# Performance work log

Hardware: AMD Instinct MI355X
Metric: run time of the kernel (lower is better)

The kernel has to match this reference:

```python
import jax, jax.numpy as jnp
import numpy as np

G = 7          # grid size
OBJ_P = 0.3    # fraction of cells containing an object


def _to_xyxy(x, y, w, h, m, n):
    # x pairs with grid index m (dim 2), y with n (dim 3), per the original loop
    cx = (x + m) / G
    cy = (y + n) / G
    return cx - w / 2, cy - h / 2, cx + w / 2, cy + h / 2


def _iou(b1, b2):
    x1a, y1a, x2a, y2a = b1
    x1b, y1b, x2b, y2b = b2
    iw = jnp.maximum(jnp.minimum(x2a, x2b) - jnp.maximum(x1a, x1b), 0.0)
    ih = jnp.maximum(jnp.minimum(y2a, y2b) - jnp.maximum(y1a, y1b), 0.0)
    inter = iw * ih
    a1 = (x2a - x1a) * (y2a - y1a)
    a2 = (x2b - x1b) * (y2b - y1b)
    union = a1 + a2 - inter
    return jnp.where(inter > 0, inter / union, 0.0)


def setup_inputs() -> dict:
    key = jax.random.key(0)
    k1, k2, k3 = jax.random.split(key, 3)
    B = 32768
    pred = jax.random.uniform(k1, (B, 30, G, G), dtype=jnp.float32)
    labels = jax.random.uniform(k2, (B, 30, G, G), dtype=jnp.float32)
    obj_mask = jax.random.bernoulli(k3, OBJ_P, (B, G, G)).astype(jnp.float32)
    labels = labels.at[:, 4].set(obj_mask)
    return {"pred": pred, "labels": labels}


def reference(pred, labels):
    B = pred.shape[0]
    m = jnp.arange(G, dtype=pred.dtype)[:, None]   # dim 2
    n = jnp.arange(G, dtype=pred.dtype)[None, :]   # dim 3

    obj = labels[:, 4] == 1.0                       # (B,G,G)

    box1 = _to_xyxy(pred[:, 0], pred[:, 1], pred[:, 2], pred[:, 3], m, n)
    box2 = _to_xyxy(pred[:, 5], pred[:, 6], pred[:, 7], pred[:, 8], m, n)
    boxg = _to_xyxy(labels[:, 0], labels[:, 1], labels[:, 2], labels[:, 3], m, n)

    iou1 = _iou(box1, boxg)
    iou2 = _iou(box2, boxg)
    resp1 = iou1 >= iou2

    coor1 = 5.0 * (jnp.sum((pred[:, 0:2] - labels[:, 0:2]) ** 2, axis=1)
                   + jnp.sum((jnp.sqrt(pred[:, 2:4]) - jnp.sqrt(labels[:, 2:4])) ** 2, axis=1))
    coor2 = 5.0 * (jnp.sum((pred[:, 5:7] - labels[:, 5:7]) ** 2, axis=1)
                   + jnp.sum((jnp.sqrt(pred[:, 7:9]) - jnp.sqrt(labels[:, 7:9])) ** 2, axis=1))

    loss_b1 = coor1 + (pred[:, 4] - iou1) ** 2 + 0.5 * (pred[:, 9] - iou2) ** 2
    loss_b2 = coor2 + (pred[:, 9] - iou2) ** 2 + 0.5 * (pred[:, 4] - iou1) ** 2

    cls = jnp.sum((pred[:, 10:] - labels[:, 10:]) ** 2, axis=1)

    obj_loss = jnp.where(resp1, loss_b1, loss_b2) + cls
    noobj_loss = 0.5 * (pred[:, 4] ** 2 + pred[:, 9] ** 2)

    total = jnp.sum(jnp.where(obj, obj_loss, noobj_loss))
    return total / B
```

## Files before the change

kernel.cpp:

```cpp
#include <hip/hip_runtime.h>


#define GRID 7
#define NCH 30
#define CPI (GRID * GRID)
#define FPI (NCH * CPI)
#define NBLK 2048

__device__ __forceinline__ float iou_xyxy(float x1a, float y1a, float x2a, float y2a,
                                          float x1b, float y1b, float x2b, float y2b) {
    float iw = fmaxf(fminf(x2a, x2b) - fmaxf(x1a, x1b), 0.0f);
    float ih = fmaxf(fminf(y2a, y2b) - fmaxf(y1a, y1b), 0.0f);
    float inter = iw * ih;
    float a1 = (x2a - x1a) * (y2a - y1a);
    float a2 = (x2b - x1b) * (y2b - y1b);
    float uni = a1 + a2 - inter;
    return inter > 0.0f ? inter / uni : 0.0f;
}

__global__ void __launch_bounds__(256) yolo_partial_kernel(
        const float* __restrict__ pred,
        const float* __restrict__ labels,
        float* __restrict__ partials,
        int ncells, float invB) {
    float acc = 0.0f;
    int stride = gridDim.x * blockDim.x;
    for (int idx = blockIdx.x * blockDim.x + threadIdx.x; idx < ncells; idx += stride) {
        int b = idx / CPI;
        int cell = idx - b * CPI;
        int m = cell / GRID;
        int n = cell - m * GRID;

        const float* pb = pred   + (size_t)b * FPI + cell;
        const float* lb = labels + (size_t)b * FPI + cell;

        float p0 = pb[0 * CPI], p1 = pb[1 * CPI], p2 = pb[2 * CPI], p3 = pb[3 * CPI];
        float p4 = pb[4 * CPI], p5 = pb[5 * CPI], p6 = pb[6 * CPI], p7 = pb[7 * CPI];
        float p8 = pb[8 * CPI], p9 = pb[9 * CPI];
        float l0 = lb[0 * CPI], l1 = lb[1 * CPI], l2 = lb[2 * CPI], l3 = lb[3 * CPI];
        float lobj = lb[4 * CPI];
        float l5 = lb[5 * CPI], l6 = lb[6 * CPI], l7 = lb[7 * CPI], l8 = lb[8 * CPI];

        float cls = 0.0f;
        #pragma unroll
        for (int c = 10; c < NCH; ++c) {
            float d = pb[c * CPI] - lb[c * CPI];
            cls += d * d;
        }

        const float inv_g = 1.0f / (float)GRID;
        float fm = (float)m, fn = (float)n;

        float cx = (p0 + fm) * inv_g, cy = (p1 + fn) * inv_g;
        float b1x1 = cx - p2 * 0.5f, b1y1 = cy - p3 * 0.5f;
        float b1x2 = cx + p2 * 0.5f, b1y2 = cy + p3 * 0.5f;
        cx = (p5 + fm) * inv_g; cy = (p6 + fn) * inv_g;
        float b2x1 = cx - p7 * 0.5f, b2y1 = cy - p8 * 0.5f;
        float b2x2 = cx + p7 * 0.5f, b2y2 = cy + p8 * 0.5f;
        cx = (l0 + fm) * inv_g; cy = (l1 + fn) * inv_g;
        float gx1 = cx - l2 * 0.5f, gy1 = cy - l3 * 0.5f;
        float gx2 = cx + l2 * 0.5f, gy2 = cy + l3 * 0.5f;

        float iou1 = iou_xyxy(b1x1, b1y1, b1x2, b1y2, gx1, gy1, gx2, gy2);
        float iou2 = iou_xyxy(b2x1, b2y1, b2x2, b2y2, gx1, gy1, gx2, gy2);
        bool resp1 = iou1 >= iou2;

        float dx = p0 - l0, dy = p1 - l1;
        float dw = sqrtf(p2) - sqrtf(l2), dh = sqrtf(p3) - sqrtf(l3);
        float coor1 = 5.0f * (dx * dx + dy * dy + dw * dw + dh * dh);
        dx = p5 - l5; dy = p6 - l6;
        dw = sqrtf(p7) - sqrtf(l7); dh = sqrtf(p8) - sqrtf(l8);
        float coor2 = 5.0f * (dx * dx + dy * dy + dw * dw + dh * dh);

        float e1 = p4 - iou1, e2 = p9 - iou2;
        float loss_b1 = coor1 + e1 * e1 + 0.5f * e2 * e2;
        float loss_b2 = coor2 + e2 * e2 + 0.5f * e1 * e1;

        float obj_loss = (resp1 ? loss_b1 : loss_b2) + cls;
        float noobj_loss = 0.5f * (p4 * p4 + p9 * p9);

        acc += ((lobj == 1.0f) ? obj_loss : noobj_loss) * invB;
    }

    #pragma unroll
    for (int off = 32; off > 0; off >>= 1)
        acc += __shfl_down(acc, off, 64);

    __shared__ float rsm[4];
    int lane = threadIdx.x & 63;
    int wid = threadIdx.x >> 6;
    if (lane == 0) rsm[wid] = acc;
    __syncthreads();
    if (threadIdx.x == 0)
        partials[blockIdx.x] = rsm[0] + rsm[1] + rsm[2] + rsm[3];
}

__global__ void __launch_bounds__(256) yolo_final_kernel(
        const float* __restrict__ partials, float* __restrict__ out, int n) {
    float acc = 0.0f;
    for (int i = threadIdx.x; i < n; i += 256)
        acc += partials[i];
    #pragma unroll
    for (int off = 32; off > 0; off >>= 1)
        acc += __shfl_down(acc, off, 64);
    __shared__ float rsm[4];
    int lane = threadIdx.x & 63;
    int wid = threadIdx.x >> 6;
    if (lane == 0) rsm[wid] = acc;
    __syncthreads();
    if (threadIdx.x == 0)
        out[0] = rsm[0] + rsm[1] + rsm[2] + rsm[3];
}

extern "C" void kernel_launch(void* const* d_in, const int* in_sizes, int n_in,
                              void* d_out, int out_size, void* d_ws, size_t ws_size,
                              hipStream_t stream) {
    const float* pred = (const float*)d_in[0];
    const float* labels = (const float*)d_in[1];
    float* out = (float*)d_out;
    float* partials = (float*)d_ws;

    int total = in_sizes[0];
    int B = total / FPI;
    int ncells = B * CPI;

    yolo_partial_kernel<<<NBLK, 256, 0, stream>>>(pred, labels, partials,
                                                  ncells, 1.0f / (float)B);
    yolo_final_kernel<<<1, 256, 0, stream>>>(partials, out, NBLK);
}
```

Baseline: 386.4 us.

## Stage per-image tiles into LDS with direct global-to-LDS vector loads

Each block now handles groups of 4 images. It first copies the contiguous pred and label slabs into shared memory with 16-byte global_load_lds transfers. The per-cell loss is then computed from LDS, replacing the 39 strided scalar global loads each thread issued before. Leftover images that do not fill a group are handled in the final reduction kernel, which now sums one partial per group. The cost is about 47KB of LDS per block, which limits occupancy, and roughly a quarter of each block's threads sit idle during compute with no overlap between loading and computing.

```diff
diff --git a/kernel.cpp b/kernel.cpp
--- a/kernel.cpp
+++ b/kernel.cpp
@@ -5,7 +5,15 @@
 #define NCH 30
 #define CPI (GRID * GRID)
 #define FPI (NCH * CPI)
-#define NBLK 2048
+#define IPB 4
+#define BLK 256
+#define CELLS_PB (IPB * CPI)
+#define F_PB (IPB * FPI)
+#define F4_PB (F_PB / 4)
+#define FALLBACK_NBLK 2048
+
+typedef const __attribute__((address_space(1))) void gvoid_t;
+typedef __attribute__((address_space(3))) void lvoid_t;
 
 __device__ __forceinline__ float iou_xyxy(float x1a, float y1a, float x2a, float y2a,
                                           float x1b, float y1b, float x2b, float y2b) {
@@ -18,68 +26,90 @@
     return inter > 0.0f ? inter / uni : 0.0f;
 }
 
-__global__ void __launch_bounds__(256) yolo_partial_kernel(
+__device__ __forceinline__ float cell_loss(const float* __restrict__ pb,
+                                           const float* __restrict__ lb,
+                                           float fm, float fn) {
+    float p0 = pb[0 * CPI], p1 = pb[1 * CPI], p2 = pb[2 * CPI], p3 = pb[3 * CPI];
+    float p4 = pb[4 * CPI], p5 = pb[5 * CPI], p6 = pb[6 * CPI], p7 = pb[7 * CPI];
+    float p8 = pb[8 * CPI], p9 = pb[9 * CPI];
+    float l0 = lb[0 * CPI], l1 = lb[1 * CPI], l2 = lb[2 * CPI], l3 = lb[3 * CPI];
+    float lobj = lb[4 * CPI];
+    float l5 = lb[5 * CPI], l6 = lb[6 * CPI], l7 = lb[7 * CPI], l8 = lb[8 * CPI];
+
+    float cls = 0.0f;
+    #pragma unroll
+    for (int c = 10; c < NCH; ++c) {
+        float d = pb[c * CPI] - lb[c * CPI];
+        cls += d * d;
+    }
+
+    const float inv_g = 1.0f / (float)GRID;
+
+    float cx = (p0 + fm) * inv_g, cy = (p1 + fn) * inv_g;
+    float b1x1 = cx - p2 * 0.5f, b1y1 = cy - p3 * 0.5f;
+    float b1x2 = cx + p2 * 0.5f, b1y2 = cy + p3 * 0.5f;
+    cx = (p5 + fm) * inv_g; cy = (p6 + fn) * inv_g;
+    float b2x1 = cx - p7 * 0.5f, b2y1 = cy - p8 * 0.5f;
+    float b2x2 = cx + p7 * 0.5f, b2y2 = cy + p8 * 0.5f;
+    cx = (l0 + fm) * inv_g; cy = (l1 + fn) * inv_g;
+    float gx1 = cx - l2 * 0.5f, gy1 = cy - l3 * 0.5f;
+    float gx2 = cx + l2 * 0.5f, gy2 = cy + l3 * 0.5f;
+
+    float iou1 = iou_xyxy(b1x1, b1y1, b1x2, b1y2, gx1, gy1, gx2, gy2);
+    float iou2 = iou_xyxy(b2x1, b2y1, b2x2, b2y2, gx1, gy1, gx2, gy2);
+    bool resp1 = iou1 >= iou2;
+
+    float dx = p0 - l0, dy = p1 - l1;
+    float dw = sqrtf(p2) - sqrtf(l2), dh = sqrtf(p3) - sqrtf(l3);
+    float coor1 = 5.0f * (dx * dx + dy * dy + dw * dw + dh * dh);
+    dx = p5 - l5; dy = p6 - l6;
+    dw = sqrtf(p7) - sqrtf(l7); dh = sqrtf(p8) - sqrtf(l8);
+    float coor2 = 5.0f * (dx * dx + dy * dy + dw * dw + dh * dh);
+
+    float e1 = p4 - iou1, e2 = p9 - iou2;
+    float loss_b1 = coor1 + e1 * e1 + 0.5f * e2 * e2;
+    float loss_b2 = coor2 + e2 * e2 + 0.5f * e1 * e1;
+
+    float obj_loss = (resp1 ? loss_b1 : loss_b2) + cls;
+    float noobj_loss = 0.5f * (p4 * p4 + p9 * p9);
+
+    return (lobj == 1.0f) ? obj_loss : noobj_loss;
+}
+
+__global__ void __launch_bounds__(BLK) yolo_partial_kernel(
         const float* __restrict__ pred,
         const float* __restrict__ labels,
         float* __restrict__ partials,
-        int ncells, float invB) {
+        int ngroups, float invB) {
+    __shared__ __align__(16) float sp[F_PB];
+    __shared__ __align__(16) float sl[F_PB];
+
     float acc = 0.0f;
-    int stride = gridDim.x * blockDim.x;
-    for (int idx = blockIdx.x * blockDim.x + threadIdx.x; idx < ncells; idx += stride) {
-        int b = idx / CPI;
-        int cell = idx - b * CPI;
-        int m = cell / GRID;
-        int n = cell - m * GRID;
 
-        const float* pb = pred   + (size_t)b * FPI + cell;
-        const float* lb = labels + (size_t)b * FPI + cell;
+    for (int g = blockIdx.x; g < ngroups; g += gridDim.x) {
+        const float* gp = pred   + (size_t)g * F_PB;
+        const float* gl = labels + (size_t)g * F_PB;
 
-        float p0 = pb[0 * CPI], p1 = pb[1 * CPI], p2 = pb[2 * CPI], p3 = pb[3 * CPI];
-        float p4 = pb[4 * CPI], p5 = pb[5 * CPI], p6 = pb[6 * CPI], p7 = pb[7 * CPI];
-        float p8 = pb[8 * CPI], p9 = pb[9 * CPI];
-        float l0 = lb[0 * CPI], l1 = lb[1 * CPI], l2 = lb[2 * CPI], l3 = lb[3 * CPI];
-        float lobj = lb[4 * CPI];
-        float l5 = lb[5 * CPI], l6 = lb[6 * CPI], l7 = lb[7 * CPI], l8 = lb[8 * CPI];
+        for (int j = threadIdx.x; j < F4_PB; j += BLK)
+            __builtin_amdgcn_global_load_lds((gvoid_t*)(gp + 4 * j),
+                                             (lvoid_t*)(sp + 4 * j), 16, 0, 0);
+        for (int j = threadIdx.x; j < F4_PB; j += BLK)
+            __builtin_amdgcn_global_load_lds((gvoid_t*)(gl + 4 * j),
+                                             (lvoid_t*)(sl + 4 * j), 16, 0, 0);
 
-        float cls = 0.0f;
-        #pragma unroll
-        for (int c = 10; c < NCH; ++c) {
-            float d = pb[c * CPI] - lb[c * CPI];
-            cls += d * d;
+        asm volatile("s_waitcnt vmcnt(0)" ::: "memory");
+        __syncthreads();
+
+        int t = threadIdx.x;
+        if (t < CELLS_PB) {
+            int i = t / CPI;
+            int cell = t - i * CPI;
+            int m = cell / GRID;
+            int n = cell - m * GRID;
+            acc += cell_loss(&sp[i * FPI + cell], &sl[i * FPI + cell],
+                             (float)m, (float)n) * invB;
         }
-
-        const float inv_g = 1.0f / (float)GRID;
-        float fm = (float)m, fn = (float)n;
-
-        float cx = (p0 + fm) * inv_g, cy = (p1 + fn) * inv_g;
-        float b1x1 = cx - p2 * 0.5f, b1y1 = cy - p3 * 0.5f;
-        float b1x2 = cx + p2 * 0.5f, b1y2 = cy + p3 * 0.5f;
-        cx = (p5 + fm) * inv_g; cy = (p6 + fn) * inv_g;
-        float b2x1 = cx - p7 * 0.5f, b2y1 = cy - p8 * 0.5f;
-        float b2x2 = cx + p7 * 0.5f, b2y2 = cy + p8 * 0.5f;
-        cx = (l0 + fm) * inv_g; cy = (l1 + fn) * inv_g;
-        float gx1 = cx - l2 * 0.5f, gy1 = cy - l3 * 0.5f;
-        float gx2 = cx + l2 * 0.5f, gy2 = cy + l3 * 0.5f;
-
-        float iou1 = iou_xyxy(b1x1, b1y1, b1x2, b1y2, gx1, gy1, gx2, gy2);
-        float iou2 = iou_xyxy(b2x1, b2y1, b2x2, b2y2, gx1, gy1, gx2, gy2);
-        bool resp1 = iou1 >= iou2;
-
-        float dx = p0 - l0, dy = p1 - l1;
-        float dw = sqrtf(p2) - sqrtf(l2), dh = sqrtf(p3) - sqrtf(l3);
-        float coor1 = 5.0f * (dx * dx + dy * dy + dw * dw + dh * dh);
-        dx = p5 - l5; dy = p6 - l6;
-        dw = sqrtf(p7) - sqrtf(l7); dh = sqrtf(p8) - sqrtf(l8);
-        float coor2 = 5.0f * (dx * dx + dy * dy + dw * dw + dh * dh);
-
-        float e1 = p4 - iou1, e2 = p9 - iou2;
-        float loss_b1 = coor1 + e1 * e1 + 0.5f * e2 * e2;
-        float loss_b2 = coor2 + e2 * e2 + 0.5f * e1 * e1;
-
-        float obj_loss = (resp1 ? loss_b1 : loss_b2) + cls;
-        float noobj_loss = 0.5f * (p4 * p4 + p9 * p9);
-
-        acc += ((lobj == 1.0f) ? obj_loss : noobj_loss) * invB;
+        __syncthreads();
     }
 
     #pragma unroll
@@ -96,10 +126,24 @@
 }
 
 __global__ void __launch_bounds__(256) yolo_final_kernel(
-        const float* __restrict__ partials, float* __restrict__ out, int n) {
+        const float* __restrict__ partials, int np,
+        const float* __restrict__ pred, const float* __restrict__ labels,
+        int b0, int B, float invB, float* __restrict__ out) {
     float acc = 0.0f;
-    for (int i = threadIdx.x; i < n; i += 256)
+    for (int i = threadIdx.x; i < np; i += 256)
         acc += partials[i];
+
+    int remcells = (B - b0) * CPI;
+    for (int idx = threadIdx.x; idx < remcells; idx += 256) {
+        int b = b0 + idx / CPI;
+        int cell = idx % CPI;
+        int m = cell / GRID;
+        int n = cell - m * GRID;
+        acc += cell_loss(pred + (size_t)b * FPI + cell,
+                         labels + (size_t)b * FPI + cell,
+                         (float)m, (float)n) * invB;
+    }
+
     #pragma unroll
     for (int off = 32; off > 0; off >>= 1)
         acc += __shfl_down(acc, off, 64);
@@ -122,9 +166,20 @@
 
     int total = in_sizes[0];
     int B = total / FPI;
-    int ncells = B * CPI;
+    if (B <= 0) return;
+    float invB = 1.0f / (float)B;
+    int ngroups = B / IPB;
+    int b0 = ngroups * IPB;
 
-    yolo_partial_kernel<<<NBLK, 256, 0, stream>>>(pred, labels, partials,
-                                                  ncells, 1.0f / (float)B);
-    yolo_final_kernel<<<1, 256, 0, stream>>>(partials, out, NBLK);
+    int nblk = ngroups;
+    if (ngroups == 0) {
+        nblk = 1;
+    } else if ((size_t)ngroups * sizeof(float) > ws_size) {
+        nblk = (ngroups < FALLBACK_NBLK) ? ngroups : FALLBACK_NBLK;
+    }
+
+    yolo_partial_kernel<<<nblk, BLK, 0, stream>>>(pred, labels, partials,
+                                                  ngroups, invB);
+    yolo_final_kernel<<<1, 256, 0, stream>>>(partials, nblk, pred, labels,
+                                             b0, B, invB, out);
 }
```

Result: no change. 379.8 us (median of 2 runs) (-1.7%).

## Split class loss into separate vectorized float4 streaming kernel

Applied to the files above, without the earlier changes.

Moves the class-channel squared-error sum into its own kernel that streams pred and labels with float4 loads over the whole tensor. Each element looks up the object mask with a gather and skips the non-class channels. The per-cell kernel now reads only the first ten channels, and both kernels write partial sums that one final kernel reduces. The cost targeted is the strided, uncoalesced per-cell reads of the 20 class channels. In exchange the box channels are read twice, the vector loads pull in non-class data, every class element does an extra mask gather, and there is one more kernel launch.

```diff
diff --git a/kernel.cpp b/kernel.cpp
--- a/kernel.cpp
+++ b/kernel.cpp
@@ -3,9 +3,13 @@
 
 #define GRID 7
 #define NCH 30
-#define CPI (GRID * GRID)
-#define FPI (NCH * CPI)
-#define NBLK 2048
+#define CPI 49
+#define FPI 1470
+#define CH_CLS0 490
+#define OBJ_OFF 196
+#define NBLK_A 2048
+#define NBLK_B 2048
+#define BLK 256
 
 __device__ __forceinline__ float iou_xyxy(float x1a, float y1a, float x2a, float y2a,
                                           float x1b, float y1b, float x2b, float y2b) {
@@ -18,21 +22,78 @@
     return inter > 0.0f ? inter / uni : 0.0f;
 }
 
-__global__ void __launch_bounds__(256) yolo_partial_kernel(
+__device__ __forceinline__ void block_reduce_write(float acc, float* dst) {
+    #pragma unroll
+    for (int off = 32; off > 0; off >>= 1)
+        acc += __shfl_down(acc, off, 64);
+    __shared__ float rsm[4];
+    int lane = threadIdx.x & 63;
+    int wid = threadIdx.x >> 6;
+    if (lane == 0) rsm[wid] = acc;
+    __syncthreads();
+    if (threadIdx.x == 0)
+        dst[blockIdx.x] = rsm[0] + rsm[1] + rsm[2] + rsm[3];
+}
+
+__global__ void __launch_bounds__(BLK) yolo_cls_kernel(
+        const float* __restrict__ pred,
+        const float* __restrict__ labels,
+        float* __restrict__ partials,
+        int nElem, float invB) {
+    float acc = 0.0f;
+    int nf4 = nElem >> 2;
+    int stride = gridDim.x * blockDim.x;
+    const float4* p4 = reinterpret_cast<const float4*>(pred);
+    const float4* l4 = reinterpret_cast<const float4*>(labels);
+
+    for (int i = blockIdx.x * blockDim.x + threadIdx.x; i < nf4; i += stride) {
+        float4 pv = p4[i];
+        float4 lv = l4[i];
+        int e0 = i << 2;
+        float pe[4] = {pv.x, pv.y, pv.z, pv.w};
+        float le[4] = {lv.x, lv.y, lv.z, lv.w};
+        #pragma unroll
+        for (int k = 0; k < 4; ++k) {
+            int e = e0 + k;
+            int img = e / FPI;
+            int r = e - img * FPI;
+            if (r >= CH_CLS0) {
+                int cell = r % CPI;
+                float o = labels[img * FPI + OBJ_OFF + cell];
+                float d = pe[k] - le[k];
+                acc += (o == 1.0f) ? d * d : 0.0f;
+            }
+        }
+    }
+    if (blockIdx.x == 0 && threadIdx.x < (nElem & 3)) {
+        int e = (nf4 << 2) + threadIdx.x;
+        int img = e / FPI;
+        int r = e - img * FPI;
+        if (r >= CH_CLS0) {
+            int cell = r % CPI;
+            float o = labels[img * FPI + OBJ_OFF + cell];
+            float d = pred[e] - labels[e];
+            if (o == 1.0f) acc += d * d;
+        }
+    }
+    block_reduce_write(acc * invB, partials);
+}
+
+__global__ void __launch_bounds__(BLK) yolo_cell_kernel(
         const float* __restrict__ pred,
         const float* __restrict__ labels,
         float* __restrict__ partials,
         int ncells, float invB) {
     float acc = 0.0f;
     int stride = gridDim.x * blockDim.x;
-    for (int idx = blockIdx.x * blockDim.x + threadIdx.x; idx < ncells; idx += stride) {
-        int b = idx / CPI;
-        int cell = idx - b * CPI;
+    for (int t = blockIdx.x * blockDim.x + threadIdx.x; t < ncells; t += stride) {
+        int img = t / CPI;
+        int cell = t - img * CPI;
         int m = cell / GRID;
         int n = cell - m * GRID;
 
-        const float* pb = pred   + (size_t)b * FPI + cell;
-        const float* lb = labels + (size_t)b * FPI + cell;
+        const float* pb = pred + img * FPI + cell;
+        const float* lb = labels + img * FPI + cell;
 
         float p0 = pb[0 * CPI], p1 = pb[1 * CPI], p2 = pb[2 * CPI], p3 = pb[3 * CPI];
         float p4 = pb[4 * CPI], p5 = pb[5 * CPI], p6 = pb[6 * CPI], p7 = pb[7 * CPI];
@@ -40,13 +101,6 @@
         float l0 = lb[0 * CPI], l1 = lb[1 * CPI], l2 = lb[2 * CPI], l3 = lb[3 * CPI];
         float lobj = lb[4 * CPI];
         float l5 = lb[5 * CPI], l6 = lb[6 * CPI], l7 = lb[7 * CPI], l8 = lb[8 * CPI];
-
-        float cls = 0.0f;
-        #pragma unroll
-        for (int c = 10; c < NCH; ++c) {
-            float d = pb[c * CPI] - lb[c * CPI];
-            cls += d * d;
-        }
 
         const float inv_g = 1.0f / (float)GRID;
         float fm = (float)m, fn = (float)n;
@@ -76,29 +130,18 @@
         float loss_b1 = coor1 + e1 * e1 + 0.5f * e2 * e2;
         float loss_b2 = coor2 + e2 * e2 + 0.5f * e1 * e1;
 
-        float obj_loss = (resp1 ? loss_b1 : loss_b2) + cls;
+        float obj_loss = resp1 ? loss_b1 : loss_b2;
         float noobj_loss = 0.5f * (p4 * p4 + p9 * p9);
 
-        acc += ((lobj == 1.0f) ? obj_loss : noobj_loss) * invB;
+        acc += (lobj == 1.0f) ? obj_loss : noobj_loss;
     }
-
-    #pragma unroll
-    for (int off = 32; off > 0; off >>= 1)
-        acc += __shfl_down(acc, off, 64);
-
-    __shared__ float rsm[4];
-    int lane = threadIdx.x & 63;
-    int wid = threadIdx.x >> 6;
-    if (lane == 0) rsm[wid] = acc;
-    __syncthreads();
-    if (threadIdx.x == 0)
-        partials[blockIdx.x] = rsm[0] + rsm[1] + rsm[2] + rsm[3];
+    block_reduce_write(acc * invB, partials);
 }
 
 __global__ void __launch_bounds__(256) yolo_final_kernel(
-        const float* __restrict__ partials, float* __restrict__ out, int n) {
+        const float* __restrict__ partials, float* __restrict__ out, int np) {
     float acc = 0.0f;
-    for (int i = threadIdx.x; i < n; i += 256)
+    for (int i = threadIdx.x; i < np; i += 256)
         acc += partials[i];
     #pragma unroll
     for (int off = 32; off > 0; off >>= 1)
@@ -122,9 +165,19 @@
 
     int total = in_sizes[0];
     int B = total / FPI;
+    if (B <= 0) return;
+    float invB = 1.0f / (float)B;
     int ncells = B * CPI;
 
-    yolo_partial_kernel<<<NBLK, 256, 0, stream>>>(pred, labels, partials,
-                                                  ncells, 1.0f / (float)B);
-    yolo_final_kernel<<<1, 256, 0, stream>>>(partials, out, NBLK);
+    int na = NBLK_A, nb = NBLK_B;
+    size_t cap = ws_size / sizeof(float);
+    if ((size_t)(na + nb) > cap) {
+        na = (int)(cap / 2) > 0 ? (int)(cap / 2) : 1;
+        nb = na;
+    }
+
+    yolo_cls_kernel<<<na, BLK, 0, stream>>>(pred, labels, partials, total, invB);
+    yolo_cell_kernel<<<nb, BLK, 0, stream>>>(pred, labels, partials + na,
+                                             ncells, invB);
+    yolo_final_kernel<<<1, 256, 0, stream>>>(partials, out, na + nb);
 }
```

After: 402.2 us. 1.04x slower.
